# Kernel tuning notes

Hardware: AMD Instinct MI355X
Metric: run time of the kernel (lower is better)

## Reference

```python
import jax, jax.numpy as jnp
import numpy as np

HIDDEN = 3584
H = 28          # num attention heads
KV = 4          # num key-value heads
HD = 128        # head dim
MROPE = [16, 24, 24]  # sum*2 == HD
EPS = 1e-6
S_TOT = 4096
N_SAMPLES = 4


def rmsnorm(x, w, eps=EPS):
    return x * jax.lax.rsqrt(jnp.mean(x * x, axis=-1, keepdims=True) + eps) * w


def rotate_half(x):
    x1, x2 = jnp.split(x, 2, axis=-1)
    return jnp.concatenate([-x2, x1], axis=-1)


def mrope_merge(t):
    # t: [3, S, HD] -> [S, HD], section i taken from rope axis i%3
    cuts = np.cumsum(np.array(MROPE) * 2)[:-1]
    parts = jnp.split(t, cuts, axis=-1)
    return jnp.concatenate([p[i % 3] for i, p in enumerate(parts)], axis=-1)


def setup_inputs() -> dict:
    key = jax.random.key(0)
    ks = iter(jax.random.split(key, 32))
    std = 0.02

    def w(shape):
        return jax.random.normal(next(ks), shape, dtype=jnp.float32) * std

    inp = {
        "packed_sequence": jax.random.normal(next(ks), (S_TOT, HIDDEN), dtype=jnp.float32),
        "packed_cos": jax.random.uniform(next(ks), (3, S_TOT, HD), dtype=jnp.float32, minval=-1.0, maxval=1.0),
        "packed_sin": jax.random.uniform(next(ks), (3, S_TOT, HD), dtype=jnp.float32, minval=-1.0, maxval=1.0),
    }
    # und / geo indices partition [0, S_TOT)
    inp["packed_und_token_indexes"] = jnp.arange(S_TOT // 2, dtype=jnp.int64 if jax.config.jax_enable_x64 else jnp.int32)
    inp["packed_geo_token_indexes"] = jnp.arange(S_TOT // 2, dtype=inp["packed_und_token_indexes"].dtype) + S_TOT // 2
    inp["sample_len"] = S_TOT // N_SAMPLES

    for tag in ("und", "geo"):
        inp[f"q_w_{tag}"] = w((H * HD, HIDDEN))
        inp[f"q_b_{tag}"] = jnp.zeros((H * HD,), jnp.float32)
        inp[f"k_w_{tag}"] = w((KV * HD, HIDDEN))
        inp[f"k_b_{tag}"] = jnp.zeros((KV * HD,), jnp.float32)
        inp[f"v_w_{tag}"] = w((KV * HD, HIDDEN))
        inp[f"v_b_{tag}"] = jnp.zeros((KV * HD,), jnp.float32)
        inp[f"o_w_{tag}"] = w((HIDDEN, H * HD))
        inp[f"q_norm_{tag}"] = jnp.ones((HD,), jnp.float32)
        inp[f"k_norm_{tag}"] = jnp.ones((HD,), jnp.float32)
    return inp


def reference(packed_sequence, packed_cos, packed_sin,
              q_w_und, q_b_und, k_w_und, k_b_und, v_w_und, v_b_und, o_w_und,
              q_norm_und, k_norm_und,
              q_w_geo, q_b_geo, k_w_geo, k_b_geo, v_w_geo, v_b_geo, o_w_geo,
              q_norm_geo, k_norm_geo,
              packed_und_token_indexes, packed_geo_token_indexes, sample_len):
    S, D = packed_sequence.shape
    G = H // KV
    und, geo = packed_und_token_indexes, packed_geo_token_indexes
    xu = packed_sequence[und]
    xg = packed_sequence[geo]

    def scatter(dim, fu, fg):
        out = jnp.zeros((S, dim), packed_sequence.dtype)
        return out.at[und].set(fu).at[geo].set(fg)

    # modality-routed QKV projections (gather -> gemm -> scatter)
    q = scatter(H * HD, xu @ q_w_und.T + q_b_und, xg @ q_w_geo.T + q_b_geo).reshape(S, H, HD)
    k = scatter(KV * HD, xu @ k_w_und.T + k_b_und, xg @ k_w_geo.T + k_b_geo).reshape(S, KV, HD)
    v = scatter(KV * HD, xu @ v_w_und.T + v_b_und, xg @ v_w_geo.T + v_b_geo).reshape(S, KV, HD)

    # per-modality QK RMSNorm
    qn = jnp.zeros_like(q).at[und].set(rmsnorm(q[und], q_norm_und)).at[geo].set(rmsnorm(q[geo], q_norm_geo))
    kn = jnp.zeros_like(k).at[und].set(rmsnorm(k[und], k_norm_und)).at[geo].set(rmsnorm(k[geo], k_norm_geo))

    # multimodal rotary embedding
    cos = mrope_merge(packed_cos)[:, None, :]  # [S,1,HD]
    sin = mrope_merge(packed_sin)[:, None, :]
    qr = qn * cos + rotate_half(qn) * sin
    kr = kn * cos + rotate_half(kn) * sin

    # block-diagonal causal attention over packed equal-length samples
    L = int(sample_len)
    B = S // L
    qb = qr.reshape(B, L, H, HD)
    kb = jnp.repeat(kr.reshape(B, L, KV, HD), G, axis=2)  # GQA expansion
    vb = jnp.repeat(v.reshape(B, L, KV, HD), G, axis=2)
    scores = jnp.einsum('blhd,bmhd->bhlm', qb, kb) / np.sqrt(HD).astype(np.float32)
    causal = jnp.tril(jnp.ones((L, L), bool))
    scores = jnp.where(causal, scores, jnp.finfo(scores.dtype).min)
    attn = jax.nn.softmax(scores, axis=-1)
    out = jnp.einsum('bhlm,bmhd->blhd', attn, vb).reshape(S, H * HD)

    # modality-routed output projection
    res = jnp.zeros((S, D), packed_sequence.dtype)
    res = res.at[und].set(out[und] @ o_w_und.T).at[geo].set(out[geo] @ o_w_geo.T)
    return res
```

## Files before the change

### kernel.cpp

```cpp
#include <hip/hip_runtime.h>
#include <hip/hip_bf16.h>
#include <stdint.h>

#define HIDDEN 3584
#define NH 28
#define NKV 4
#define HD 128
#define GQ (NH / NKV)
#define NQKV ((NH + 2 * NKV) * HD)
#define LSAMP 1024

typedef __bf16 bf16x8 __attribute__((ext_vector_type(8)));
typedef float f32x4 __attribute__((ext_vector_type(4)));

__device__ __forceinline__ unsigned short f2bf(float f) {
  unsigned int u = __float_as_uint(f);
  u += 0x7fffu + ((u >> 16) & 1u);
  return (unsigned short)(u >> 16);
}
__device__ __forceinline__ float bf2f(unsigned short h) {
  return __uint_as_float(((unsigned int)h) << 16);
}

__device__ __forceinline__ void gload16(const void* g, void* l) {
  __builtin_amdgcn_global_load_lds(
      (const __attribute__((address_space(1))) void*)g,
      (__attribute__((address_space(3))) void*)l, 16, 0, 0);
}

__global__ void build_maps_kernel(const int* __restrict__ und, const int* __restrict__ geo,
                                  int nu, int ng,
                                  int* __restrict__ row_of_token, int* __restrict__ tok_of_row,
                                  int* __restrict__ mod_of_token) {
  int i = blockIdx.x * 256 + threadIdx.x;
  if (i < nu) {
    int t = und[i];
    row_of_token[t] = i; tok_of_row[i] = t; mod_of_token[t] = 0;
  } else if (i < nu + ng) {
    int j = i - nu;
    int t = geo[j];
    row_of_token[t] = nu + j; tok_of_row[nu + j] = t; mod_of_token[t] = 1;
  }
}

struct Cvt8 {
  const float* src[8];
  unsigned short* dst[8];
  int cum[8];
};
__global__ void convert8_kernel(Cvt8 a, int tot4) {
  int i = blockIdx.x * blockDim.x + threadIdx.x;
  const int stride = gridDim.x * blockDim.x;
  for (; i < tot4; i += stride) {
    int seg = 0;
#pragma unroll
    for (int s2 = 1; s2 < 8; ++s2) seg += (i >= a.cum[s2]);
    const int off = i - a.cum[seg];
    float4 v = reinterpret_cast<const float4*>(a.src[seg])[off];
    reinterpret_cast<ushort4*>(a.dst[seg])[off] =
        make_ushort4(f2bf(v.x), f2bf(v.y), f2bf(v.z), f2bf(v.w));
  }
}

__global__ void gather_x_kernel(const float* __restrict__ X, const int* __restrict__ tok_of_row,
                                unsigned short* __restrict__ Xg) {
  const int r = blockIdx.x;
  const int tok = tok_of_row[r];
  const float4* src = reinterpret_cast<const float4*>(X + (size_t)tok * HIDDEN);
  ushort4* dst = reinterpret_cast<ushort4*>(Xg + (size_t)r * HIDDEN);
  for (int i = threadIdx.x; i < HIDDEN / 4; i += 256) {
    float4 v = src[i];
    dst[i] = make_ushort4(f2bf(v.x), f2bf(v.y), f2bf(v.z), f2bf(v.w));
  }
}

template <int OUTMODE, int WR, int WC, int NF>
__global__ __launch_bounds__(512, 2)
void gemm2_kernel(const unsigned short* __restrict__ A,
                  const unsigned short* __restrict__ W0, const unsigned short* __restrict__ W1,
                  const float* __restrict__ qb0, const float* __restrict__ kb0, const float* __restrict__ vb0,
                  const float* __restrict__ qb1, const float* __restrict__ kb1, const float* __restrict__ vb1,
                  unsigned short* __restrict__ Obf, float* __restrict__ Of32,
                  const int* __restrict__ tok_of_row,
                  int nu, int ng, int N, int K, int NX, int NY) {
  constexpr int MF = 256 / WR / 16;
  constexpr int BN = WC * NF * 16;
  constexpr int BUFSZ = 32768 + BN * 128;
  constexpr int BCH = BN * 8;
  __shared__ char lds[2 * BUFSZ];

  const int nwg = NX * NY * 2;
  int id = blockIdx.x + NX * (blockIdx.y + NY * blockIdx.z);
  {
    const int q = nwg >> 3, r = nwg & 7;
    const int xcd = id & 7, pos = id >> 3;
    id = (xcd < r ? xcd * (q + 1) : r * (q + 1) + (xcd - r) * q) + pos;
  }
  const int bx = id % NX;
  const int byz = id / NX;
  const int by = byz % NY;
  const int bz = byz / NY;

  const int baseRow = bz ? nu : 0;
  const int Mcount = bz ? ng : nu;
  const int mbase = by * 256;
  if (mbase >= Mcount) return;
  const unsigned short* W = bz ? W1 : W0;

  const int t = threadIdx.x;
  const int w = t >> 6, l = t & 63;
  const int l15 = l & 15, l4 = l >> 4;
  const int wr = w / WC, wc = w % WC;
  const int wrr = wr * (MF * 16), wcc = wc * (NF * 16);
  const int ncol0 = bx * BN;

  f32x4 acc[MF][NF] = {};

  const int nk = K >> 6;

  auto stage = [&](int bufIdx, int kt) {
    char* base = lds + bufIdx * BUFSZ;
    const int k0 = kt * 64;
#pragma unroll
    for (int i = 0; i < 4; ++i) {
      const int c = t + i * 512;
      const int row = c >> 3, slot = c & 7;
      const int srck = (slot ^ (row & 7)) << 3;
      int ar = mbase + row; if (ar >= Mcount) ar = Mcount - 1;
      gload16(A + (size_t)(baseRow + ar) * K + k0 + srck, base + c * 16);
    }
#pragma unroll
    for (int i = 0; i < 4; ++i) {
      const int c = t + i * 512;
      const int row = c >> 3, slot = c & 7;
      const int srck = (slot ^ (row & 7)) << 3;
      gload16(W + (size_t)(ncol0 + row) * K + k0 + srck, base + 32768 + c * 16);
    }
    if (BCH > 2048) {
      if (t < BCH - 2048) {
        const int c = t + 2048;
        const int row = c >> 3, slot = c & 7;
        const int srck = (slot ^ (row & 7)) << 3;
        gload16(W + (size_t)(ncol0 + row) * K + k0 + srck, base + 32768 + c * 16);
      }
    }
  };

  stage(0, 0);
  asm volatile("s_waitcnt vmcnt(0)\n\ts_barrier" ::: "memory");

  for (int kt = 0; kt < nk; ++kt) {
    char* Ab = lds + (kt & 1) * BUFSZ;
    char* Bb = Ab + 32768;

    if (kt + 1 < nk) stage((kt + 1) & 1, kt + 1);

#pragma unroll
    for (int ks = 0; ks < 2; ++ks) {
      bf16x8 af[MF], bfr[NF];
#pragma unroll
      for (int mf = 0; mf < MF; ++mf) {
        const int row = wrr + mf * 16 + l15;
        af[mf] = *reinterpret_cast<const bf16x8*>(Ab + row * 128 + (((ks * 4 + l4) ^ (row & 7)) << 4));
      }
#pragma unroll
      for (int nf = 0; nf < NF; ++nf) {
        const int row = wcc + nf * 16 + l15;
        bfr[nf] = *reinterpret_cast<const bf16x8*>(Bb + row * 128 + (((ks * 4 + l4) ^ (row & 7)) << 4));
      }
      __builtin_amdgcn_s_setprio(1);
#pragma unroll
      for (int mf = 0; mf < MF; ++mf)
#pragma unroll
        for (int nf = 0; nf < NF; ++nf)
          acc[mf][nf] = __builtin_amdgcn_mfma_f32_16x16x32_bf16(af[mf], bfr[nf], acc[mf][nf], 0, 0, 0);
      __builtin_amdgcn_s_setprio(0);
    }

    if (kt + 1 < nk) {
      asm volatile("s_waitcnt vmcnt(0)\n\ts_barrier" ::: "memory");
    }
  }

#pragma unroll
  for (int mf = 0; mf < MF; ++mf) {
#pragma unroll
    for (int rr = 0; rr < 4; ++rr) {
      const int ml = mbase + wrr + mf * 16 + l4 * 4 + rr;
      if (ml >= Mcount) continue;
      int trow = 0;
      if (OUTMODE == 1) trow = tok_of_row[baseRow + ml];
#pragma unroll
      for (int nf = 0; nf < NF; ++nf) {
        const int n = ncol0 + wcc + nf * 16 + l15;
        const float v = acc[mf][nf][rr];
        if (OUTMODE == 0) {
          const float* qb = bz ? qb1 : qb0;
          const float* kb = bz ? kb1 : kb0;
          const float* vb = bz ? vb1 : vb0;
          const float bias = (n < NH * HD) ? qb[n]
                              : ((n < (NH + NKV) * HD) ? kb[n - NH * HD] : vb[n - (NH + NKV) * HD]);
          Obf[(size_t)(baseRow + ml) * N + n] = f2bf(v + bias);
        } else {
          Of32[(size_t)trow * N + n] = v;
        }
      }
    }
  }
}

__global__ __launch_bounds__(64)
void norm_rope_kernel(const unsigned short* __restrict__ Y,
                      const int* __restrict__ row_of_token, const int* __restrict__ mod_of_token,
                      const float* __restrict__ pcos, const float* __restrict__ psin,
                      const float* __restrict__ qn_u, const float* __restrict__ kn_u,
                      const float* __restrict__ qn_g, const float* __restrict__ kn_g,
                      unsigned short* __restrict__ Qr,
                      unsigned short* __restrict__ Kr,
                      unsigned short* __restrict__ Vt,
                      int S) {
  const int s = blockIdx.x, t = threadIdx.x;
  const int r = row_of_token[s];
  const int m = mod_of_token[s];
  const float* qn = m ? qn_g : qn_u;
  const float* kn = m ? kn_g : kn_u;
  const int d0 = t, d1 = t + 64;
  const int a0 = (d0 < 32) ? 0 : (d0 < 80 ? 1 : 2);
  const int a1 = (d1 < 80) ? 1 : 2;
  const float c0 = pcos[((size_t)a0 * S + s) * HD + d0];
  const float c1 = pcos[((size_t)a1 * S + s) * HD + d1];
  const float s0 = psin[((size_t)a0 * S + s) * HD + d0];
  const float s1 = psin[((size_t)a1 * S + s) * HD + d1];
  const float qnw0 = qn[t], qnw1 = qn[t + 64];
  const float knw0 = kn[t], knw1 = kn[t + 64];
  const unsigned short* yrow = Y + (size_t)r * NQKV;
  constexpr float SC = 0.08838834764831845f;

#pragma unroll 4
  for (int hh = 0; hh < NH; ++hh) {
    float x0 = bf2f(yrow[hh * HD + t]);
    float x1 = bf2f(yrow[hh * HD + t + 64]);
    float ss = x0 * x0 + x1 * x1;
#pragma unroll
    for (int dd = 1; dd < 64; dd <<= 1) ss += __shfl_xor(ss, dd);
    const float rs = rsqrtf(ss * (1.f / 128.f) + 1e-6f);
    const float q0 = x0 * rs * qnw0, q1 = x1 * rs * qnw1;
    unsigned short* dst = Qr + ((size_t)hh * S + s) * HD;
    dst[t] = f2bf((q0 * c0 - q1 * s0) * SC);
    dst[t + 64] = f2bf((q1 * c1 + q0 * s1) * SC);
  }
#pragma unroll
  for (int kh = 0; kh < NKV; ++kh) {
    float x0 = bf2f(yrow[NH * HD + kh * HD + t]);
    float x1 = bf2f(yrow[NH * HD + kh * HD + t + 64]);
    float ss = x0 * x0 + x1 * x1;
#pragma unroll
    for (int dd = 1; dd < 64; dd <<= 1) ss += __shfl_xor(ss, dd);
    const float rs = rsqrtf(ss * (1.f / 128.f) + 1e-6f);
    const float k0 = x0 * rs * knw0, k1 = x1 * rs * knw1;
    unsigned short* dst = Kr + ((size_t)kh * S + s) * HD;
    dst[t] = f2bf(k0 * c0 - k1 * s0);
    dst[t + 64] = f2bf(k1 * c1 + k0 * s1);
  }
#pragma unroll
  for (int vh = 0; vh < NKV; ++vh) {
    float x0 = bf2f(yrow[(NH + NKV) * HD + vh * HD + t]);
    float x1 = bf2f(yrow[(NH + NKV) * HD + vh * HD + t + 64]);
    Vt[((size_t)(vh * HD + t)) * S + s] = f2bf(x0);
    Vt[((size_t)(vh * HD + t + 64)) * S + s] = f2bf(x1);
  }
}

__global__ __launch_bounds__(256, 2)
void attn_kernel(const unsigned short* __restrict__ Qr, const unsigned short* __restrict__ Kr,
                 const unsigned short* __restrict__ Vt, const int* __restrict__ row_of_token,
                 unsigned short* __restrict__ Og, int S) {
  __shared__ char lds[16384 + 16384 + 64 * 144];
  char* Klds = lds;
  char* Vlds = lds + 16384;
  char* Plds = lds + 32768;
  const int qt = blockIdx.x, h = blockIdx.y, b = blockIdx.z;
  const int kvh = h / GQ;
  const int t = threadIdx.x, w = t >> 6, l = t & 63;
  const int l15 = l & 15, l4 = l >> 4;
  const int sbase = b * LSAMP;

  bf16x8 aq[4];
  {
    const int qrow = sbase + qt * 64 + w * 16 + l15;
    const unsigned short* qp = Qr + ((size_t)h * S + qrow) * HD + l4 * 8;
#pragma unroll
    for (int kk = 0; kk < 4; ++kk) aq[kk] = *reinterpret_cast<const bf16x8*>(qp + kk * 32);
  }
  f32x4 acc[8] = {};
  float mr[4] = {-INFINITY, -INFINITY, -INFINITY, -INFINITY};
  float lr[4] = {0.f, 0.f, 0.f, 0.f};

  for (int kt = 0; kt <= qt; ++kt) {
    const int kb0 = sbase + kt * 64;
#pragma unroll
    for (int i = 0; i < 4; ++i) {
      const int c = t + i * 256;
      const int row = c >> 4, slot = c & 15;
      const int srcs = slot ^ (row & 15);
      gload16(Kr + ((size_t)kvh * S + kb0 + row) * HD + srcs * 8, Klds + c * 16);
    }
#pragma unroll
    for (int i = 0; i < 4; ++i) {
      const int c = t + i * 256;
      const int row = c >> 3, slot = c & 7;
      const int srcs = slot ^ (row & 7);
      gload16(Vt + (size_t)(kvh * HD + row) * S + kb0 + srcs * 8, Vlds + c * 16);
    }
    __syncthreads();

    f32x4 sa[4] = {};
#pragma unroll
    for (int kk = 0; kk < 4; ++kk) {
      bf16x8 bk[4];
#pragma unroll
      for (int nf = 0; nf < 4; ++nf) {
        const int row = nf * 16 + l15;
        const int slot = kk * 4 + l4;
        bk[nf] = *reinterpret_cast<const bf16x8*>(Klds + row * 256 + ((slot ^ (row & 15)) << 4));
      }
#pragma unroll
      for (int nf = 0; nf < 4; ++nf)
        sa[nf] = __builtin_amdgcn_mfma_f32_16x16x32_bf16(aq[kk], bk[nf], sa[nf], 0, 0, 0);
    }
    const int qg = qt * 64 + w * 16 + l4 * 4;
#pragma unroll
    for (int nf = 0; nf < 4; ++nf) {
      const int cg = kt * 64 + nf * 16 + l15;
#pragma unroll
      for (int rr = 0; rr < 4; ++rr)
        if (cg > qg + rr) sa[nf][rr] = -INFINITY;
    }
    float mnew[4], psum[4], pv[4][4];
#pragma unroll
    for (int rr = 0; rr < 4; ++rr) {
      float mx = fmaxf(fmaxf(sa[0][rr], sa[1][rr]), fmaxf(sa[2][rr], sa[3][rr]));
      mx = fmaxf(mx, mr[rr]);
#pragma unroll
      for (int dd = 1; dd < 16; dd <<= 1) mx = fmaxf(mx, __shfl_xor(mx, dd));
      mnew[rr] = mx;
      float sum = 0.f;
#pragma unroll
      for (int nf = 0; nf < 4; ++nf) {
        const float p = __expf(sa[nf][rr] - mx);
        pv[nf][rr] = p;
        sum += p;
      }
#pragma unroll
      for (int dd = 1; dd < 16; dd <<= 1) sum += __shfl_xor(sum, dd);
      psum[rr] = sum;
    }
#pragma unroll
    for (int rr = 0; rr < 4; ++rr) {
      const float alpha = __expf(mr[rr] - mnew[rr]);
      lr[rr] = lr[rr] * alpha + psum[rr];
      mr[rr] = mnew[rr];
#pragma unroll
      for (int nf2 = 0; nf2 < 8; ++nf2) acc[nf2][rr] *= alpha;
    }
#pragma unroll
    for (int rr = 0; rr < 4; ++rr) {
      const int row = w * 16 + l4 * 4 + rr;
#pragma unroll
      for (int nf = 0; nf < 4; ++nf)
        ((unsigned short*)(Plds + row * 144))[nf * 16 + l15] = f2bf(pv[nf][rr]);
    }
    __syncthreads();
#pragma unroll
    for (int kk2 = 0; kk2 < 2; ++kk2) {
      const bf16x8 ap = *reinterpret_cast<const bf16x8*>(Plds + (w * 16 + l15) * 144 + kk2 * 64 + l4 * 16);
#pragma unroll
      for (int nf2 = 0; nf2 < 8; ++nf2) {
        const int rowd = nf2 * 16 + l15;
        const int slot = kk2 * 4 + l4;
        const bf16x8 bv = *reinterpret_cast<const bf16x8*>(Vlds + rowd * 128 + ((slot ^ (rowd & 7)) << 4));
        acc[nf2] = __builtin_amdgcn_mfma_f32_16x16x32_bf16(ap, bv, acc[nf2], 0, 0, 0);
      }
    }
    __syncthreads();
  }

  const int srow0 = sbase + qt * 64 + w * 16 + l4 * 4;
#pragma unroll
  for (int rr = 0; rr < 4; ++rr) {
    const float inv = 1.f / lr[rr];
    const int mrow = row_of_token[srow0 + rr];
    unsigned short* orow = Og + (size_t)mrow * (NH * HD) + h * HD;
#pragma unroll
    for (int nf2 = 0; nf2 < 8; ++nf2) orow[nf2 * 16 + l15] = f2bf(acc[nf2][rr] * inv);
  }
}

extern "C" void kernel_launch(void* const* d_in, const int* in_sizes, int n_in,
                              void* d_out, int out_size, void* d_ws, size_t ws_size,
                              hipStream_t stream) {
  const float* X = (const float*)d_in[0];
  const float* pcos = (const float*)d_in[1];
  const float* psin = (const float*)d_in[2];
  const int* und = (const int*)d_in[3];
  const int* geo = (const int*)d_in[4];
  const int nu = in_sizes[3], ng = in_sizes[4];
  const int S = in_sizes[0] / HIDDEN;

  const float* qw[2] = {(const float*)d_in[6], (const float*)d_in[15]};
  const float* qb[2] = {(const float*)d_in[7], (const float*)d_in[16]};
  const float* kw[2] = {(const float*)d_in[8], (const float*)d_in[17]};
  const float* kb[2] = {(const float*)d_in[9], (const float*)d_in[18]};
  const float* vw[2] = {(const float*)d_in[10], (const float*)d_in[19]};
  const float* vb[2] = {(const float*)d_in[11], (const float*)d_in[20]};
  const float* ow[2] = {(const float*)d_in[12], (const float*)d_in[21]};
  const float* qn[2] = {(const float*)d_in[13], (const float*)d_in[22]};
  const float* kn[2] = {(const float*)d_in[14], (const float*)d_in[23]};

  char* ws = (char*)d_ws;
  size_t off = 0;
  auto alloc = [&](size_t bytes) {
    char* p = ws + off;
    off = (off + bytes + 255) & ~(size_t)255;
    return p;
  };
  int* row_of_token = (int*)alloc((size_t)S * 4);
  int* tok_of_row = (int*)alloc((size_t)S * 4);
  int* mod_of_token = (int*)alloc((size_t)S * 4);
  unsigned short* Wqkv[2] = {(unsigned short*)alloc((size_t)NQKV * HIDDEN * 2),
                             (unsigned short*)alloc((size_t)NQKV * HIDDEN * 2)};
  unsigned short* Wo[2] = {(unsigned short*)alloc((size_t)HIDDEN * HIDDEN * 2),
                           (unsigned short*)alloc((size_t)HIDDEN * HIDDEN * 2)};
  unsigned short* Xg = (unsigned short*)alloc((size_t)S * HIDDEN * 2);
  unsigned short* Yqkv = (unsigned short*)alloc((size_t)S * NQKV * 2);
  unsigned short* Qr = (unsigned short*)alloc((size_t)NH * S * HD * 2);
  unsigned short* Kr = (unsigned short*)alloc((size_t)NKV * S * HD * 2);
  unsigned short* Vt = (unsigned short*)alloc((size_t)NKV * S * HD * 2);
  unsigned short* Og = (unsigned short*)alloc((size_t)S * NH * HD * 2);
  (void)ws_size; (void)n_in; (void)out_size;

  build_maps_kernel<<<(S + 255) / 256, 256, 0, stream>>>(und, geo, nu, ng,
                                                         row_of_token, tok_of_row, mod_of_token);
  {
    Cvt8 ca;
    const float* srcs[8] = {qw[0], kw[0], vw[0], ow[0], qw[1], kw[1], vw[1], ow[1]};
    unsigned short* dsts[8] = {
        Wqkv[0], Wqkv[0] + (size_t)NH * HD * HIDDEN, Wqkv[0] + (size_t)(NH + NKV) * HD * HIDDEN, Wo[0],
        Wqkv[1], Wqkv[1] + (size_t)NH * HD * HIDDEN, Wqkv[1] + (size_t)(NH + NKV) * HD * HIDDEN, Wo[1]};
    const int n4s[8] = {NH * HD * HIDDEN / 4, NKV * HD * HIDDEN / 4, NKV * HD * HIDDEN / 4, HIDDEN * HIDDEN / 4,
                        NH * HD * HIDDEN / 4, NKV * HD * HIDDEN / 4, NKV * HD * HIDDEN / 4, HIDDEN * HIDDEN / 4};
    int cum = 0;
    for (int i = 0; i < 8; ++i) { ca.src[i] = srcs[i]; ca.dst[i] = dsts[i]; ca.cum[i] = cum; cum += n4s[i]; }
    convert8_kernel<<<2048, 256, 0, stream>>>(ca, cum);
  }
  gather_x_kernel<<<S, 256, 0, stream>>>(X, tok_of_row, Xg);

  const int maxM = (nu > ng ? nu : ng);
  {
    const int NX = NQKV / 288, NY = (maxM + 255) / 256;
    gemm2_kernel<0, 4, 2, 9><<<dim3(NX, NY, 2), 512, 0, stream>>>(
        Xg, Wqkv[0], Wqkv[1], qb[0], kb[0], vb[0], qb[1], kb[1], vb[1],
        Yqkv, nullptr, nullptr, nu, ng, NQKV, HIDDEN, NX, NY);
  }

  norm_rope_kernel<<<S, 64, 0, stream>>>(Yqkv, row_of_token, mod_of_token, pcos, psin,
                                         qn[0], kn[0], qn[1], kn[1], Qr, Kr, Vt, S);

  attn_kernel<<<dim3(LSAMP / 64, NH, S / LSAMP), 256, 0, stream>>>(Qr, Kr, Vt, row_of_token, Og, S);

  {
    const int NX = HIDDEN / 256, NY = (maxM + 255) / 256;
    gemm2_kernel<1, 2, 4, 4><<<dim3(NX, NY, 2), 512, 0, stream>>>(
        Og, Wo[0], Wo[1], nullptr, nullptr, nullptr, nullptr, nullptr, nullptr,
        nullptr, (float*)d_out, tok_of_row, nu, ng, HIDDEN, HIDDEN, NX, NY);
  }
}
```

Measured before the change: 466.4 us.

## Double-buffer K/V tiles in attention, schedule heavy query tiles first, defer row-sum reduction

Attention now double-buffers the K and V tiles in LDS, so the next tile's global loads are issued while the current tile's MFMAs run. It also drops two block-wide barriers per iteration by relying on each wave reading only its own rows of the P buffer. Query tiles are launched in reverse order so the longest causal rows start first, which should even out the tail. The per-row sum shuffle reduction is moved out of the loop and done once at the end. LDS per block roughly doubles, which may cut occupancy, and gload16 is likely asynchronous, so the vmcnt-based wait has to match how it is implemented.

Result: no change. 467.3 us (+0.2%).

```diff
diff --git a/kernel.cpp b/kernel.cpp
--- a/kernel.cpp
+++ b/kernel.cpp
@@ -274,12 +274,11 @@
 __global__ __launch_bounds__(256, 2)
 void attn_kernel(const unsigned short* __restrict__ Qr, const unsigned short* __restrict__ Kr,
                  const unsigned short* __restrict__ Vt, const int* __restrict__ row_of_token,
-                 unsigned short* __restrict__ Og, int S) {
-  __shared__ char lds[16384 + 16384 + 64 * 144];
-  char* Klds = lds;
-  char* Vlds = lds + 16384;
-  char* Plds = lds + 32768;
-  const int qt = blockIdx.x, h = blockIdx.y, b = blockIdx.z;
+                 unsigned short* __restrict__ Og, int S, int NXQ) {
+  __shared__ char lds[2 * 16384 + 2 * 16384 + 64 * 144];
+  char* Plds = lds + 65536;
+  const int qt = NXQ - 1 - blockIdx.x;
+  const int h = blockIdx.y, b = blockIdx.z;
   const int kvh = h / GQ;
   const int t = threadIdx.x, w = t >> 6, l = t & 63;
   const int l15 = l & 15, l4 = l >> 4;
@@ -296,23 +295,34 @@
   float mr[4] = {-INFINITY, -INFINITY, -INFINITY, -INFINITY};
   float lr[4] = {0.f, 0.f, 0.f, 0.f};
 
-  for (int kt = 0; kt <= qt; ++kt) {
+  auto stage = [&](int bufIdx, int kt) {
+    char* Kb = lds + bufIdx * 16384;
+    char* Vb = lds + 32768 + bufIdx * 16384;
     const int kb0 = sbase + kt * 64;
 #pragma unroll
     for (int i = 0; i < 4; ++i) {
       const int c = t + i * 256;
       const int row = c >> 4, slot = c & 15;
       const int srcs = slot ^ (row & 15);
-      gload16(Kr + ((size_t)kvh * S + kb0 + row) * HD + srcs * 8, Klds + c * 16);
+      gload16(Kr + ((size_t)kvh * S + kb0 + row) * HD + srcs * 8, Kb + c * 16);
     }
 #pragma unroll
     for (int i = 0; i < 4; ++i) {
       const int c = t + i * 256;
       const int row = c >> 3, slot = c & 7;
       const int srcs = slot ^ (row & 7);
-      gload16(Vt + (size_t)(kvh * HD + row) * S + kb0 + srcs * 8, Vlds + c * 16);
-    }
-    __syncthreads();
+      gload16(Vt + (size_t)(kvh * HD + row) * S + kb0 + srcs * 8, Vb + c * 16);
+    }
+  };
+
+  stage(0, 0);
+  asm volatile("s_waitcnt vmcnt(0)\n\ts_barrier" ::: "memory");
+
+  for (int kt = 0; kt <= qt; ++kt) {
+    char* Kb = lds + (kt & 1) * 16384;
+    char* Vb = lds + 32768 + (kt & 1) * 16384;
+
+    if (kt < qt) stage((kt + 1) & 1, kt + 1);
 
     f32x4 sa[4] = {};
 #pragma unroll
@@ -322,12 +332,13 @@
       for (int nf = 0; nf < 4; ++nf) {
         const int row = nf * 16 + l15;
         const int slot = kk * 4 + l4;
-        bk[nf] = *reinterpret_cast<const bf16x8*>(Klds + row * 256 + ((slot ^ (row & 15)) << 4));
+        bk[nf] = *reinterpret_cast<const bf16x8*>(Kb + row * 256 + ((slot ^ (row & 15)) << 4));
       }
 #pragma unroll
       for (int nf = 0; nf < 4; ++nf)
         sa[nf] = __builtin_amdgcn_mfma_f32_16x16x32_bf16(aq[kk], bk[nf], sa[nf], 0, 0, 0);
     }
+
     const int qg = qt * 64 + w * 16 + l4 * 4;
 #pragma unroll
     for (int nf = 0; nf < 4; ++nf) {
@@ -336,33 +347,28 @@
       for (int rr = 0; rr < 4; ++rr)
         if (cg > qg + rr) sa[nf][rr] = -INFINITY;
     }
-    float mnew[4], psum[4], pv[4][4];
+
+    float pv[4][4];
 #pragma unroll
     for (int rr = 0; rr < 4; ++rr) {
       float mx = fmaxf(fmaxf(sa[0][rr], sa[1][rr]), fmaxf(sa[2][rr], sa[3][rr]));
       mx = fmaxf(mx, mr[rr]);
 #pragma unroll
       for (int dd = 1; dd < 16; dd <<= 1) mx = fmaxf(mx, __shfl_xor(mx, dd));
-      mnew[rr] = mx;
-      float sum = 0.f;
+      const float alpha = __expf(mr[rr] - mx);
+      mr[rr] = mx;
+      float part = 0.f;
 #pragma unroll
       for (int nf = 0; nf < 4; ++nf) {
         const float p = __expf(sa[nf][rr] - mx);
         pv[nf][rr] = p;
-        sum += p;
-      }
-#pragma unroll
-      for (int dd = 1; dd < 16; dd <<= 1) sum += __shfl_xor(sum, dd);
-      psum[rr] = sum;
-    }
-#pragma unroll
-    for (int rr = 0; rr < 4; ++rr) {
-      const float alpha = __expf(mr[rr] - mnew[rr]);
-      lr[rr] = lr[rr] * alpha + psum[rr];
-      mr[rr] = mnew[rr];
+        part += p;
+      }
+      lr[rr] = lr[rr] * alpha + part;
 #pragma unroll
       for (int nf2 = 0; nf2 < 8; ++nf2) acc[nf2][rr] *= alpha;
     }
+
 #pragma unroll
     for (int rr = 0; rr < 4; ++rr) {
       const int row = w * 16 + l4 * 4 + rr;
@@ -370,7 +376,7 @@
       for (int nf = 0; nf < 4; ++nf)
         ((unsigned short*)(Plds + row * 144))[nf * 16 + l15] = f2bf(pv[nf][rr]);
     }
-    __syncthreads();
+
 #pragma unroll
     for (int kk2 = 0; kk2 < 2; ++kk2) {
       const bf16x8 ap = *reinterpret_cast<const bf16x8*>(Plds + (w * 16 + l15) * 144 + kk2 * 64 + l4 * 16);
@@ -378,12 +384,20 @@
       for (int nf2 = 0; nf2 < 8; ++nf2) {
         const int rowd = nf2 * 16 + l15;
         const int slot = kk2 * 4 + l4;
-        const bf16x8 bv = *reinterpret_cast<const bf16x8*>(Vlds + rowd * 128 + ((slot ^ (rowd & 7)) << 4));
+        const bf16x8 bv = *reinterpret_cast<const bf16x8*>(Vb + rowd * 128 + ((slot ^ (rowd & 7)) << 4));
         acc[nf2] = __builtin_amdgcn_mfma_f32_16x16x32_bf16(ap, bv, acc[nf2], 0, 0, 0);
       }
     }
-    __syncthreads();
-  }
+
+    if (kt < qt) {
+      asm volatile("s_waitcnt vmcnt(0)\n\ts_barrier" ::: "memory");
+    }
+  }
+
+#pragma unroll
+  for (int rr = 0; rr < 4; ++rr)
+#pragma unroll
+    for (int dd = 1; dd < 16; dd <<= 1) lr[rr] += __shfl_xor(lr[rr], dd);
 
   const int srow0 = sbase + qt * 64 + w * 16 + l4 * 4;
 #pragma unroll
@@ -466,7 +480,10 @@
   norm_rope_kernel<<<S, 64, 0, stream>>>(Yqkv, row_of_token, mod_of_token, pcos, psin,
                                          qn[0], kn[0], qn[1], kn[1], Qr, Kr, Vt, S);
 
-  attn_kernel<<<dim3(LSAMP / 64, NH, S / LSAMP), 256, 0, stream>>>(Qr, Kr, Vt, row_of_token, Og, S);
+  {
+    const int NXQ = LSAMP / 64;
+    attn_kernel<<<dim3(NXQ, NH, S / LSAMP), 256, 0, stream>>>(Qr, Kr, Vt, row_of_token, Og, S, NXQ);
+  }
 
   {
     const int NX = HIDDEN / 256, NY = (maxM + 255) / 256;
```
